# Optimization experiments

Measured on AMD Instinct MI355X. Metric: run time of the kernel, lower is better.

## Reference

```python
import jax, jax.numpy as jnp
import numpy as np

B, S, DIM = 4, 1024, 2048
NH, NKV, HD = 16, 4, 128
G = NH // NKV  # query heads per kv head


def _rope(t, cos, sin):
    # t: (B, S, H, HD); cos/sin: (S, HD//2). Llama-style pairwise rotation.
    tr = t.reshape(*t.shape[:-1], HD // 2, 2)
    t_r, t_i = tr[..., 0], tr[..., 1]
    c = cos[None, :, None, :]
    s = sin[None, :, None, :]
    out_r = t_r * c - t_i * s
    out_i = t_r * s + t_i * c
    return jnp.stack([out_r, out_i], axis=-1).reshape(t.shape)


def setup_inputs() -> dict:
    key = jax.random.key(0)
    ks = jax.random.split(key, 5)
    x = jax.random.normal(ks[0], (B, S, DIM), dtype=jnp.float32)
    # Standard RoPE frequencies
    inv_freq = 1.0 / (10000.0 ** (jnp.arange(0, HD, 2, dtype=jnp.float32) / HD))
    ang = jnp.outer(jnp.arange(S, dtype=jnp.float32), inv_freq)  # (S, HD//2)
    freqs_cos = jnp.cos(ang)
    freqs_sin = jnp.sin(ang)
    # Additive causal mask (1,1,S,S)
    causal = jnp.tril(jnp.ones((S, S), dtype=bool))
    attention_mask = jnp.where(causal, 0.0, -1e9).astype(jnp.float32)[None, None]
    sc = 0.02
    wq = jax.random.normal(ks[1], (NH * HD, DIM), dtype=jnp.float32) * sc
    wk = jax.random.normal(ks[2], (NKV * HD, DIM), dtype=jnp.float32) * sc
    wv = jax.random.normal(ks[3], (NKV * HD, DIM), dtype=jnp.float32) * sc
    wo = jax.random.normal(ks[4], (DIM, NH * HD), dtype=jnp.float32) * sc
    return {"x": x, "freqs_cos": freqs_cos, "freqs_sin": freqs_sin,
            "attention_mask": attention_mask, "wq": wq, "wk": wk, "wv": wv, "wo": wo}


def reference(x, freqs_cos, freqs_sin, attention_mask, wq, wk, wv, wo):
    b, s, _ = x.shape
    q = (x @ wq.T).reshape(b, s, NH, HD)
    k = (x @ wk.T).reshape(b, s, NKV, HD)
    v = (x @ wv.T).reshape(b, s, NKV, HD)
    q = _rope(q, freqs_cos, freqs_sin)
    k = _rope(k, freqs_cos, freqs_sin)
    # kv cache (pre-repeat, as in the torch module)
    new_kv_cache = (k, v)
    # GQA attention: broadcast KV heads across query-head groups instead of
    # materializing repeat_kv (identical math).
    qh = q.transpose(0, 2, 1, 3).reshape(b, NKV, G, s, HD)  # (b, kv, g, s, d)
    kh = k.transpose(0, 2, 1, 3)                             # (b, kv, s, d)
    vh = v.transpose(0, 2, 1, 3)
    scale = 1.0 / jnp.sqrt(jnp.asarray(HD, dtype=x.dtype))
    scores = jnp.einsum('bkgqd,bksd->bkgqs', qh, kh) * scale
    scores = scores + attention_mask[:, :, None]  # (1,1,1,S,S) broadcast
    attn = jax.nn.softmax(scores, axis=-1)
    out = jnp.einsum('bkgqs,bksd->bkgqd', attn, vh)
    out = out.reshape(b, NH, s, HD).transpose(0, 2, 1, 3).reshape(b, s, NH * HD)
    out = out @ wo.T
    return (out, new_kv_cache)
```

## Files before the change

### kernel.cpp

```cpp
#include <hip/hip_runtime.h>

typedef __bf16 bf16;
typedef __bf16 bf16x8 __attribute__((ext_vector_type(8)));
typedef __bf16 bf16x4 __attribute__((ext_vector_type(4)));
typedef float  f32x4  __attribute__((ext_vector_type(4)));

#define AS1 __attribute__((address_space(1)))
#define AS3 __attribute__((address_space(3)))

__device__ __forceinline__ void gload16(void* g, void* l) {
  __builtin_amdgcn_global_load_lds((AS1 void*)g, (AS3 void*)l, 16, 0, 0);
}

__global__ void cast_all(const float4* __restrict__ x,  const float4* __restrict__ wq,
                         const float4* __restrict__ wk, const float4* __restrict__ wv,
                         const float4* __restrict__ wo,
                         bf16x4* __restrict__ xb, bf16x4* __restrict__ wqb,
                         bf16x4* __restrict__ wkvb, bf16x4* __restrict__ wob) {
  long i = (long)blockIdx.x * 256 + threadIdx.x;
  float4 v; bf16x4* dp;
  if (i < 2097152)      { v = x[i];            dp = xb + i; }
  else if (i < 3145728) { v = wq[i - 2097152]; dp = wqb + (i - 2097152); }
  else if (i < 3407872) { v = wk[i - 3145728]; dp = wkvb + (i - 3145728); }
  else if (i < 3670016) { v = wv[i - 3407872]; dp = wkvb + 262144 + (i - 3407872); }
  else                  { v = wo[i - 3670016]; dp = wob + (i - 3670016); }
  bf16x4 o;
  o[0] = (bf16)v.x; o[1] = (bf16)v.y; o[2] = (bf16)v.z; o[3] = (bf16)v.w;
  *dp = o;
}

#define OPEN() \
  asm volatile("s_waitcnt lgkmcnt(0)" ::: "memory"); \
  __builtin_amdgcn_sched_barrier(0); \
  __builtin_amdgcn_s_setprio(1);

#define CLOSE() \
  __builtin_amdgcn_s_setprio(0); \
  __builtin_amdgcn_sched_barrier(0); \
  __builtin_amdgcn_s_barrier();

#define WVMP() { \
  if (last) { asm volatile("s_waitcnt vmcnt(0)" ::: "memory"); } \
  else { \
    if constexpr (NFR == 3) { \
      if (w < 4) { asm volatile("s_waitcnt vmcnt(2)" ::: "memory"); } \
      else       { asm volatile("s_waitcnt vmcnt(1)" ::: "memory"); } \
    } else if constexpr (NFR == 4) { \
      asm volatile("s_waitcnt vmcnt(2)" ::: "memory"); \
    } else { \
      asm volatile("s_waitcnt vmcnt(1)" ::: "memory"); \
    } \
  } }

#define MFMAQ(q, AF, BF) \
  _Pragma("unroll") for (int kk = 0; kk < 2; kk++) \
  _Pragma("unroll") for (int m2 = 0; m2 < 2; m2++) \
  _Pragma("unroll") for (int ni = 0; ni < NFR; ni++) \
    acc[(q)*2+m2][ni] = __builtin_amdgcn_mfma_f32_16x16x32_bf16(AF[m2][kk], BF[ni][kk], acc[(q)*2+m2][ni], 0, 0, 0);

#define RD_A2(AF, buf, q) \
  AF[0][0] = rdA(buf, 2*(q),   0); AF[0][1] = rdA(buf, 2*(q),   1); \
  AF[1][0] = rdA(buf, 2*(q)+1, 0); AF[1][1] = rdA(buf, 2*(q)+1, 1);

#define RD_B(BF, buf) \
  _Pragma("unroll") for (int ni = 0; ni < NFR; ni++) { \
    BF[ni][0] = rdB(buf, ni, 0); BF[ni][1] = rdB(buf, ni, 1); }

template<int NFR>
__global__ __launch_bounds__(512, 2) void gemm8(const bf16* __restrict__ A,
                                                const bf16* __restrict__ Bt,
                                                int N, int epi,
                                                float* __restrict__ Cf,
                                                bf16* __restrict__ qbb,
                                                bf16* __restrict__ kbf,
                                                float* __restrict__ kcache,
                                                float* __restrict__ vcache,
                                                bf16* __restrict__ vtb,
                                                const float* __restrict__ fc,
                                                const float* __restrict__ fs) {
  __shared__ __align__(16) char As[2][32768];
  __shared__ __align__(16) char Bs[2][8192 * NFR];
  const int t = threadIdx.x;
  const int w = t >> 6, l = t & 63, lr = l & 15, lh = l >> 4;
  const int wr = w >> 2, wc = w & 3;
  const int m0 = blockIdx.y << 8, n0 = blockIdx.x * (NFR * 64);

  f32x4 acc[8][NFR];
#pragma unroll
  for (int i = 0; i < 8; i++)
#pragma unroll
    for (int j = 0; j < NFR; j++) acc[i][j] = {0.f, 0.f, 0.f, 0.f};

  auto stA = [&](int buf, int half, int kt) {
#pragma unroll
    for (int p = 0; p < 2; p++) {
      int c = t + (p << 9);
      int rl = c >> 3, sl = c & 7, gs = sl ^ (rl & 7);
      gload16((void*)(A + (long)(m0 + (half << 7) + rl) * 2048 + (kt << 6) + (gs << 3)),
              &As[buf][(half << 14) + (c << 4)]);
    }
  };
  auto stB = [&](int buf, int half, int kt) {
    constexpr int CH = NFR * 256;
#pragma unroll
    for (int p = 0; p < (CH + 511) >> 9; p++) {
      int c = t + (p << 9);
      if ((CH & 511) && c >= CH) continue;
      int rl = c >> 3, sl = c & 7, gs = sl ^ (rl & 7);
      gload16((void*)(Bt + (long)(n0 + half * (NFR * 32) + rl) * 2048 + (kt << 6) + (gs << 3)),
              &Bs[buf][half * (NFR * 4096) + (c << 4)]);
    }
  };
  auto rdA = [&](int buf, int mi, int kk) -> bf16x8 {
    int row = (wr << 7) + (mi << 4) + lr;
    int sl  = ((kk << 2) | lh) ^ (row & 7);
    return *(const bf16x8*)(&As[buf][row * 128 + (sl << 4)]);
  };
  auto rdB = [&](int buf, int ni, int kk) -> bf16x8 {
    int row = wc * (NFR * 16) + (ni << 4) + lr;
    int sl  = ((kk << 2) | lh) ^ (row & 7);
    return *(const bf16x8*)(&Bs[buf][row * 128 + (sl << 4)]);
  };

  bf16x8 afX[2][2], afY[2][2], bfrX[NFR][2], bfrY[NFR][2];

  stB(0, 0, 0); stB(0, 1, 0);
  stA(0, 0, 0); stA(0, 1, 0);
  stB(1, 0, 1); stB(1, 1, 1);
  if constexpr (NFR == 3) {
    if (w < 4) { asm volatile("s_waitcnt vmcnt(4)" ::: "memory"); }
    else       { asm volatile("s_waitcnt vmcnt(2)" ::: "memory"); }
  } else if constexpr (NFR == 4) {
    asm volatile("s_waitcnt vmcnt(4)" ::: "memory");
  } else {
    asm volatile("s_waitcnt vmcnt(2)" ::: "memory");
  }
  __builtin_amdgcn_s_barrier();
  RD_B(bfrX, 0);
  RD_A2(afX, 0, 0);

  const int NI = 16;
  for (int j = 0; j < NI; j++) {
    const bool last = (j == NI - 1);
    const int ktO = 2 * j + 1;

    OPEN();
    RD_A2(afY, 0, 1);
    stA(1, 0, ktO);
    MFMAQ(0, afX, bfrX); CLOSE();

    OPEN();
    RD_A2(afX, 0, 2);
    stA(1, 1, ktO);
    MFMAQ(1, afY, bfrX); CLOSE();

    OPEN();
    RD_A2(afY, 0, 3);
    if (!last) stB(0, 0, ktO + 1);
    MFMAQ(2, afX, bfrX);
    __builtin_amdgcn_s_setprio(0);
    __builtin_amdgcn_sched_barrier(0);
    WVMP();
    __builtin_amdgcn_s_barrier();

    OPEN();
    RD_B(bfrY, 1);
    RD_A2(afX, 1, 0);
    if (!last) stB(0, 1, ktO + 1);
    MFMAQ(3, afY, bfrX); CLOSE();

    OPEN();
    RD_A2(afY, 1, 1);
    if (!last) stA(0, 0, ktO + 1);
    MFMAQ(0, afX, bfrY); CLOSE();

    OPEN();
    RD_A2(afX, 1, 2);
    if (!last) stA(0, 1, ktO + 1);
    MFMAQ(1, afY, bfrY); CLOSE();

    OPEN();
    RD_A2(afY, 1, 3);
    if (!last) stB(1, 0, ktO + 2);
    MFMAQ(2, afX, bfrY);
    __builtin_amdgcn_s_setprio(0);
    __builtin_amdgcn_sched_barrier(0);
    WVMP();
    __builtin_amdgcn_s_barrier();

    OPEN();
    if (!last) {
      RD_B(bfrX, 0);
      RD_A2(afX, 0, 0);
      stB(1, 1, ktO + 2);
    }
    MFMAQ(3, afY, bfrY); CLOSE();
  }

  const float qs = 0.08838834764831845f;
  const int im = lr & 1;
#pragma unroll
  for (int mi = 0; mi < 8; mi++)
#pragma unroll
    for (int ni = 0; ni < NFR; ni++) {
      int col  = n0 + wc * (NFR * 16) + (ni << 4) + lr;
      int rowb = m0 + (wr << 7) + (mi << 4) + (lh << 2);
      if (epi == 0) {
#pragma unroll
        for (int r = 0; r < 4; r++)
          Cf[(long)(rowb + r) * N + col] = acc[mi][ni][r];
      } else if (col < 2048) {
        int i2 = (col & 127) >> 1;
#pragma unroll
        for (int r = 0; r < 4; r++) {
          int row = rowb + r, s = row & 1023;
          float c = fc[(s << 6) + i2], sn = fs[(s << 6) + i2];
          float own = acc[mi][ni][r], oth = __shfl_xor(own, 1);
          float xr = im ? oth : own, xi = im ? own : oth;
          float val = im ? (xr * sn + xi * c) : (xr * c - xi * sn);
          qbb[(long)row * 2048 + col] = (bf16)(val * qs);
        }
      } else if (col < 2560) {
        int ck = col - 2048;
        int i2 = (ck & 127) >> 1;
#pragma unroll
        for (int r = 0; r < 4; r++) {
          int row = rowb + r, s = row & 1023;
          float c = fc[(s << 6) + i2], sn = fs[(s << 6) + i2];
          float own = acc[mi][ni][r], oth = __shfl_xor(own, 1);
          float xr = im ? oth : own, xi = im ? own : oth;
          float val = im ? (xr * sn + xi * c) : (xr * c - xi * sn);
          kbf[(long)row * 512 + ck] = (bf16)val;
          kcache[(long)row * 512 + ck] = val;
        }
      } else {
        int cv = col - 2560;
        bf16x4 pk;
#pragma unroll
        for (int r = 0; r < 4; r++) {
          float v = acc[mi][ni][r];
          vcache[(long)(rowb + r) * 512 + cv] = v;
          pk[r] = (bf16)v;
        }
        int b = rowb >> 10, s0 = rowb & 1023;
        *(bf16x4*)(vtb + ((long)((b << 2) + (cv >> 7)) * 128 + (cv & 127)) * 1024 + s0) = pk;
      }
    }
}

__global__ __launch_bounds__(256) void attn_k(const bf16* __restrict__ qb,
                                              const bf16* __restrict__ kb,
                                              const bf16* __restrict__ vt,
                                              bf16* __restrict__ aob) {
  const int bh = blockIdx.x;
  const int qt = 15 - blockIdx.y;
  const int b = bh >> 4, h = bh & 15, kv = h >> 2;
  const int t = threadIdx.x, w = t >> 6, l = t & 63, lr = l & 15, lh = l >> 4;
  __shared__ __align__(16) char Ks[2][16384];
  __shared__ __align__(16) char Vs[2][16384];
  __shared__ __align__(16) bf16 Ps[4][16][72];

  bf16x8 qfrag[4];
  {
    const int qrow = (qt << 6) + (w << 4) + lr;
    const bf16* qp = qb + ((long)(b * 1024 + qrow) << 11) + (h << 7);
#pragma unroll
    for (int kc = 0; kc < 4; kc++) qfrag[kc] = *(const bf16x8*)(qp + (kc << 5) + (lh << 3));
  }

  f32x4 acc[8];
#pragma unroll
  for (int i = 0; i < 8; i++) acc[i] = {0.f, 0.f, 0.f, 0.f};
  float ls[4] = {0.f, 0.f, 0.f, 0.f};

  const bf16* kg = kb + ((long)b << 19) + (kv << 7);
  const bf16* vg = vt + ((long)(b * 4 + kv) << 17);
  const int nt = qt + 1;

  auto stage = [&](int buf, int tt2) {
    const int kv0 = tt2 << 6;
#pragma unroll
    for (int pass = 0; pass < 4; pass++) {
      int c = t + (pass << 8);
      { int row = c >> 4, slot = c & 15, gs = slot ^ (row & 7);
        gload16((void*)(kg + (long)(kv0 + row) * 512 + (gs << 3)), &Ks[buf][c * 16]); }
      { int row = c >> 3, slot = c & 7,  gs = slot ^ (row & 7);
        gload16((void*)(vg + (long)row * 1024 + kv0 + (gs << 3)), &Vs[buf][c * 16]); }
    }
  };

  stage(0, 0);
  int cur = 0;

  for (int tt = 0; tt < nt; tt++) {
    __syncthreads();
    if (tt + 1 < nt) stage(cur ^ 1, tt + 1);

    f32x4 s4[4];
#pragma unroll
    for (int nf = 0; nf < 4; nf++) s4[nf] = {0.f, 0.f, 0.f, 0.f};
    __builtin_amdgcn_s_setprio(1);
#pragma unroll
    for (int nf = 0; nf < 4; nf++) {
      int key = (nf << 4) + lr;
#pragma unroll
      for (int kc = 0; kc < 4; kc++) {
        bf16x8 kf8 = *(const bf16x8*)(&Ks[cur][0] + key * 256 + (((kc << 6) + (lh << 4)) ^ ((key & 7) << 4)));
        s4[nf] = __builtin_amdgcn_mfma_f32_16x16x32_bf16(qfrag[kc], kf8, s4[nf], 0, 0, 0);
      }
    }
    __builtin_amdgcn_s_setprio(0);

    if (tt == qt) {
      const int kv0 = tt << 6;
#pragma unroll
      for (int nf = 0; nf < 4; nf++) {
        int key = kv0 + (nf << 4) + lr;
#pragma unroll
        for (int r = 0; r < 4; r++) {
          int qg = (qt << 6) + (w << 4) + (lh << 2) + r;
          if (key > qg) s4[nf][r] = -1e30f;
        }
      }
    }

#pragma unroll
    for (int nf = 0; nf < 4; nf++)
#pragma unroll
      for (int r = 0; r < 4; r++) {
        float p = __expf(s4[nf][r] - 8.f);
        s4[nf][r] = p;
        ls[r] += p;
      }

#pragma unroll
    for (int nf = 0; nf < 4; nf++)
#pragma unroll
      for (int r = 0; r < 4; r++)
        Ps[w][(lh << 2) + r][(nf << 4) + lr] = (bf16)s4[nf][r];

    __builtin_amdgcn_s_setprio(1);
#pragma unroll
    for (int kc = 0; kc < 2; kc++) {
      bf16x8 pf8 = *(const bf16x8*)((const char*)&Ps[w][lr][0] + (kc << 6) + (lh << 4));
#pragma unroll
      for (int hf = 0; hf < 8; hf++) {
        int hd = (hf << 4) + lr;
        bf16x8 vf8 = *(const bf16x8*)(&Vs[cur][0] + hd * 128 + (((kc << 6) + (lh << 4)) ^ ((hd & 7) << 4)));
        acc[hf] = __builtin_amdgcn_mfma_f32_16x16x32_bf16(pf8, vf8, acc[hf], 0, 0, 0);
      }
    }
    __builtin_amdgcn_s_setprio(0);
    cur ^= 1;
  }

#pragma unroll
  for (int d = 1; d < 16; d <<= 1)
#pragma unroll
    for (int r = 0; r < 4; r++) ls[r] += __shfl_xor(ls[r], d);

  float inv[4];
#pragma unroll
  for (int r = 0; r < 4; r++) inv[r] = 1.f / ls[r];
#pragma unroll
  for (int hf = 0; hf < 8; hf++)
#pragma unroll
    for (int r = 0; r < 4; r++) {
      int qrow = (qt << 6) + (w << 4) + (lh << 2) + r;
      aob[((long)(b * 1024 + qrow) << 11) + (h << 7) + (hf << 4) + lr] = (bf16)(acc[hf][r] * inv[r]);
    }
}

extern "C" void kernel_launch(void* const* d_in, const int* in_sizes, int n_in,
                              void* d_out, int out_size, void* d_ws, size_t ws_size,
                              hipStream_t stream) {
  (void)in_sizes; (void)n_in; (void)out_size; (void)ws_size;
  const float* x  = (const float*)d_in[0];
  const float* fc = (const float*)d_in[1];
  const float* fs = (const float*)d_in[2];
  const float* wq = (const float*)d_in[4];
  const float* wk = (const float*)d_in[5];
  const float* wv = (const float*)d_in[6];
  const float* wo = (const float*)d_in[7];

  float* out    = (float*)d_out;
  float* kcache = out + 8388608;
  float* vcache = out + 10485760;

  char* ws = (char*)d_ws;
  bf16* xb    = (bf16*)(ws);
  bf16* wqkv  = (bf16*)(ws + 16777216);
  bf16* wob   = (bf16*)(ws + 29360128);
  bf16* qbb   = (bf16*)(ws + 54525952);
  bf16* kbf   = (bf16*)(ws + 71303168);
  bf16* vtb   = (bf16*)(ws + 75497472);
  bf16* aob   = (bf16*)(ws + 79691776);

  cast_all<<<18432, 256, 0, stream>>>((const float4*)x, (const float4*)wq,
                                      (const float4*)wk, (const float4*)wv,
                                      (const float4*)wo,
                                      (bf16x4*)xb, (bf16x4*)wqkv,
                                      (bf16x4*)(wqkv + 4194304), (bf16x4*)wob);

  gemm8<3><<<dim3(16, 16), 512, 0, stream>>>(xb, wqkv, 3072, 1, nullptr,
                                             qbb, kbf, kcache, vcache, vtb, fc, fs);

  attn_k<<<dim3(64, 16), 256, 0, stream>>>(qbb, kbf, vtb, aob);

  gemm8<2><<<dim3(16, 16), 512, 0, stream>>>(aob, wob, 2048, 0, out,
                                             nullptr, nullptr, nullptr, nullptr, nullptr,
                                             nullptr, nullptr);
}
```

Before: 160.2 us.

## Double query rows per attention block and keep P in registers via transposed MFMA

Each attention workgroup now handles 128 query rows (two 16-row fragments per wave) instead of 64, so every staged K/V tile is reused by twice as many MFMAs and the grid shrinks to 64x8. The score MFMA is computed transposed (K as A operand), so the probability fragment already matches the B-operand layout of a 16x16x16 MFMA for P·V. This removes the LDS round trip through the Ps buffer and shortens the row-sum reduction. The cost is higher register pressure from doubled accumulators, fewer workgroups for occupancy and load balance, and more causal-masking work on the two diagonal tiles.

```diff
diff --git a/kernel.cpp b/kernel.cpp
--- a/kernel.cpp
+++ b/kernel.cpp
@@ -4,6 +4,7 @@
 typedef __bf16 bf16x8 __attribute__((ext_vector_type(8)));
 typedef __bf16 bf16x4 __attribute__((ext_vector_type(4)));
 typedef float  f32x4  __attribute__((ext_vector_type(4)));
+typedef short  s16x4  __attribute__((ext_vector_type(4)));
 
 #define AS1 __attribute__((address_space(1)))
 #define AS3 __attribute__((address_space(3)))
@@ -253,29 +254,32 @@
                                               const bf16* __restrict__ vt,
                                               bf16* __restrict__ aob) {
   const int bh = blockIdx.x;
-  const int qt = 15 - blockIdx.y;
+  const int qblk = 7 - blockIdx.y;
   const int b = bh >> 4, h = bh & 15, kv = h >> 2;
   const int t = threadIdx.x, w = t >> 6, l = t & 63, lr = l & 15, lh = l >> 4;
   __shared__ __align__(16) char Ks[2][16384];
   __shared__ __align__(16) char Vs[2][16384];
-  __shared__ __align__(16) bf16 Ps[4][16][72];
-
-  bf16x8 qfrag[4];
-  {
-    const int qrow = (qt << 6) + (w << 4) + lr;
-    const bf16* qp = qb + ((long)(b * 1024 + qrow) << 11) + (h << 7);
-#pragma unroll
-    for (int kc = 0; kc < 4; kc++) qfrag[kc] = *(const bf16x8*)(qp + (kc << 5) + (lh << 3));
-  }
-
-  f32x4 acc[8];
-#pragma unroll
-  for (int i = 0; i < 8; i++) acc[i] = {0.f, 0.f, 0.f, 0.f};
-  float ls[4] = {0.f, 0.f, 0.f, 0.f};
+
+  const int rowbase = (qblk << 7) + (w << 5);
+
+  bf16x8 qfrag[2][4];
+#pragma unroll
+  for (int f = 0; f < 2; f++) {
+    const bf16* qp = qb + ((long)(b * 1024 + rowbase + (f << 4) + lr) << 11) + (h << 7);
+#pragma unroll
+    for (int kc = 0; kc < 4; kc++) qfrag[f][kc] = *(const bf16x8*)(qp + (kc << 5) + (lh << 3));
+  }
+
+  f32x4 acc[2][8];
+#pragma unroll
+  for (int f = 0; f < 2; f++)
+#pragma unroll
+    for (int i = 0; i < 8; i++) acc[f][i] = {0.f, 0.f, 0.f, 0.f};
+  float ls[2] = {0.f, 0.f};
 
   const bf16* kg = kb + ((long)b << 19) + (kv << 7);
   const bf16* vg = vt + ((long)(b * 4 + kv) << 17);
-  const int nt = qt + 1;
+  const int nt = (qblk << 1) + 2;
 
   auto stage = [&](int buf, int tt2) {
     const int kv0 = tt2 << 6;
@@ -296,79 +300,92 @@
     __syncthreads();
     if (tt + 1 < nt) stage(cur ^ 1, tt + 1);
 
-    f32x4 s4[4];
-#pragma unroll
-    for (int nf = 0; nf < 4; nf++) s4[nf] = {0.f, 0.f, 0.f, 0.f};
+    f32x4 s4[2][4];
+#pragma unroll
+    for (int f = 0; f < 2; f++)
+#pragma unroll
+      for (int nf = 0; nf < 4; nf++) s4[f][nf] = {0.f, 0.f, 0.f, 0.f};
     __builtin_amdgcn_s_setprio(1);
 #pragma unroll
     for (int nf = 0; nf < 4; nf++) {
       int key = (nf << 4) + lr;
-#pragma unroll
-      for (int kc = 0; kc < 4; kc++) {
-        bf16x8 kf8 = *(const bf16x8*)(&Ks[cur][0] + key * 256 + (((kc << 6) + (lh << 4)) ^ ((key & 7) << 4)));
-        s4[nf] = __builtin_amdgcn_mfma_f32_16x16x32_bf16(qfrag[kc], kf8, s4[nf], 0, 0, 0);
+      bf16x8 kf[4];
+#pragma unroll
+      for (int kc = 0; kc < 4; kc++)
+        kf[kc] = *(const bf16x8*)(&Ks[cur][0] + key * 256 + (((kc << 6) + (lh << 4)) ^ ((key & 7) << 4)));
+#pragma unroll
+      for (int kc = 0; kc < 4; kc++)
+        s4[0][nf] = __builtin_amdgcn_mfma_f32_16x16x32_bf16(kf[kc], qfrag[0][kc], s4[0][nf], 0, 0, 0);
+#pragma unroll
+      for (int kc = 0; kc < 4; kc++)
+        s4[1][nf] = __builtin_amdgcn_mfma_f32_16x16x32_bf16(kf[kc], qfrag[1][kc], s4[1][nf], 0, 0, 0);
+    }
+    __builtin_amdgcn_s_setprio(0);
+
+    if (tt >= (qblk << 1)) {
+      const int kv0 = tt << 6;
+#pragma unroll
+      for (int f = 0; f < 2; f++) {
+        int qg = rowbase + (f << 4) + lr;
+#pragma unroll
+        for (int nf = 0; nf < 4; nf++)
+#pragma unroll
+          for (int r = 0; r < 4; r++) {
+            int key = kv0 + (nf << 4) + (lh << 2) + r;
+            if (key > qg) s4[f][nf][r] = -1e30f;
+          }
       }
     }
-    __builtin_amdgcn_s_setprio(0);
-
-    if (tt == qt) {
-      const int kv0 = tt << 6;
+
+    s16x4 pb[2][4];
+#pragma unroll
+    for (int f = 0; f < 2; f++)
 #pragma unroll
       for (int nf = 0; nf < 4; nf++) {
-        int key = kv0 + (nf << 4) + lr;
+        bf16x4 pk;
 #pragma unroll
         for (int r = 0; r < 4; r++) {
-          int qg = (qt << 6) + (w << 4) + (lh << 2) + r;
-          if (key > qg) s4[nf][r] = -1e30f;
+          float p = __expf(s4[f][nf][r] - 8.f);
+          ls[f] += p;
+          pk[r] = (bf16)p;
         }
+        pb[f][nf] = __builtin_bit_cast(s16x4, pk);
       }
-    }
-
+
+    __builtin_amdgcn_s_setprio(1);
 #pragma unroll
     for (int nf = 0; nf < 4; nf++)
-#pragma unroll
-      for (int r = 0; r < 4; r++) {
-        float p = __expf(s4[nf][r] - 8.f);
-        s4[nf][r] = p;
-        ls[r] += p;
-      }
-
-#pragma unroll
-    for (int nf = 0; nf < 4; nf++)
-#pragma unroll
-      for (int r = 0; r < 4; r++)
-        Ps[w][(lh << 2) + r][(nf << 4) + lr] = (bf16)s4[nf][r];
-
-    __builtin_amdgcn_s_setprio(1);
-#pragma unroll
-    for (int kc = 0; kc < 2; kc++) {
-      bf16x8 pf8 = *(const bf16x8*)((const char*)&Ps[w][lr][0] + (kc << 6) + (lh << 4));
 #pragma unroll
       for (int hf = 0; hf < 8; hf++) {
         int hd = (hf << 4) + lr;
-        bf16x8 vf8 = *(const bf16x8*)(&Vs[cur][0] + hd * 128 + (((kc << 6) + (lh << 4)) ^ ((hd & 7) << 4)));
-        acc[hf] = __builtin_amdgcn_mfma_f32_16x16x32_bf16(pf8, vf8, acc[hf], 0, 0, 0);
+        bf16x4 va = *(const bf16x4*)(&Vs[cur][0] + hd * 128 +
+                      ((((nf << 1) + (lh >> 1)) ^ (lr & 7)) << 4) + ((lh & 1) << 3));
+        s16x4 vas = __builtin_bit_cast(s16x4, va);
+        acc[0][hf] = __builtin_amdgcn_mfma_f32_16x16x16bf16_1k(vas, pb[0][nf], acc[0][hf], 0, 0, 0);
+        acc[1][hf] = __builtin_amdgcn_mfma_f32_16x16x16bf16_1k(vas, pb[1][nf], acc[1][hf], 0, 0, 0);
       }
-    }
     __builtin_amdgcn_s_setprio(0);
     cur ^= 1;
   }
 
 #pragma unroll
-  for (int d = 1; d < 16; d <<= 1)
-#pragma unroll
-    for (int r = 0; r < 4; r++) ls[r] += __shfl_xor(ls[r], d);
-
-  float inv[4];
-#pragma unroll
-  for (int r = 0; r < 4; r++) inv[r] = 1.f / ls[r];
-#pragma unroll
-  for (int hf = 0; hf < 8; hf++)
-#pragma unroll
-    for (int r = 0; r < 4; r++) {
-      int qrow = (qt << 6) + (w << 4) + (lh << 2) + r;
-      aob[((long)(b * 1024 + qrow) << 11) + (h << 7) + (hf << 4) + lr] = (bf16)(acc[hf][r] * inv[r]);
-    }
+  for (int f = 0; f < 2; f++) {
+    ls[f] += __shfl_xor(ls[f], 16);
+    ls[f] += __shfl_xor(ls[f], 32);
+  }
+
+#pragma unroll
+  for (int f = 0; f < 2; f++) {
+    float inv = 1.f / ls[f];
+    long obase = ((long)(b * 1024 + rowbase + (f << 4) + lr) << 11) + (h << 7);
+#pragma unroll
+    for (int hf = 0; hf < 8; hf++) {
+      bf16x4 pk;
+#pragma unroll
+      for (int r = 0; r < 4; r++) pk[r] = (bf16)(acc[f][hf][r] * inv);
+      *(bf16x4*)(aob + obase + (hf << 4) + (lh << 2)) = pk;
+    }
+  }
 }
 
 extern "C" void kernel_launch(void* const* d_in, const int* in_sizes, int n_in,
@@ -405,7 +422,7 @@
   gemm8<3><<<dim3(16, 16), 512, 0, stream>>>(xb, wqkv, 3072, 1, nullptr,
                                              qbb, kbf, kcache, vcache, vtb, fc, fs);
 
-  attn_k<<<dim3(64, 16), 256, 0, stream>>>(qbb, kbf, vtb, aob);
+  attn_k<<<dim3(64, 8), 256, 0, stream>>>(qbb, kbf, vtb, aob);
 
   gemm8<2><<<dim3(16, 16), 512, 0, stream>>>(aob, wob, 2048, 0, out,
                                              nullptr, nullptr, nullptr, nullptr, nullptr,
```

New measurement: 177.1 us. 10.5% more time.
